# Kernel tuning notes

Measured on AMD Instinct MI355X. Metric: run time of the kernel, lower is better.

## Reference

```python
import jax, jax.numpy as jnp
import numpy as np


def conv3x3(x, w, b):
    # NCHW conv, 3x3, stride 1, pad 1
    y = jax.lax.conv_general_dilated(
        x, w, window_strides=(1, 1), padding=[(1, 1), (1, 1)],
        dimension_numbers=('NCHW', 'OIHW', 'NCHW'))
    return y + b[None, :, None, None]


def setup_inputs() -> dict:
    key = jax.random.key(0)
    ks = jax.random.split(key, 6)
    B, C, O, H, W = 4, 128, 128, 160, 160
    x = jax.random.normal(ks[0], (B, C, H, W), dtype=jnp.float32)
    # offset conv: small weights so sampling stays near the regular grid
    w_off = jax.random.normal(ks[1], (18, C, 3, 3), dtype=jnp.float32) * 0.1
    b_off = jnp.zeros((18,), dtype=jnp.float32)
    w_mask = jax.random.normal(ks[2], (9, C, 3, 3), dtype=jnp.float32) * 0.1
    b_mask = jnp.zeros((9,), dtype=jnp.float32)
    w = jax.random.normal(ks[3], (O, C, 3, 3), dtype=jnp.float32) * (1.0 / np.sqrt(C * 9))
    b = jax.random.normal(ks[4], (O,), dtype=jnp.float32) * 0.01
    return {'x': x, 'w_off': w_off, 'b_off': b_off,
            'w_mask': w_mask, 'b_mask': b_mask, 'w': w, 'b': b}


def reference(x, w_off, b_off, w_mask, b_mask, w, b):
    B, C, H, W = x.shape
    K = 9  # 3x3 kernel taps
    # offset: [B, 18, H, W] -> [B, K, 2, H, W]; channel layout is (dy, dx) per tap
    off = conv3x3(x, w_off, b_off).reshape(B, K, 2, H, W)
    dy, dx = off[:, :, 0], off[:, :, 1]                 # [B, K, H, W]
    mask = jax.nn.sigmoid(conv3x3(x, w_mask, b_mask))   # [B, K, H, W]

    # sampling positions: p = p_out - pad + k + offset  (stride 1, pad 1, dil 1)
    ky = (jnp.repeat(jnp.arange(3), 3) - 1).astype(x.dtype).reshape(1, K, 1, 1)
    kx = (jnp.tile(jnp.arange(3), 3) - 1).astype(x.dtype).reshape(1, K, 1, 1)
    hy = jnp.arange(H, dtype=x.dtype).reshape(1, 1, H, 1)
    wx = jnp.arange(W, dtype=x.dtype).reshape(1, 1, 1, W)
    py = hy + ky + dy   # [B, K, H, W]
    px = wx + kx + dx

    y0f = jnp.floor(py)
    x0f = jnp.floor(px)
    ly = py - y0f       # bilinear weights
    lx = px - x0f
    y0 = y0f.astype(jnp.int32)
    x0 = x0f.astype(jnp.int32)

    xf = x.reshape(B, C, H * W)

    def gather(iy, ix):
        # zero-padded gather at integer coords [B, K, H, W] -> [B, C, K, H, W]
        valid = ((iy >= 0) & (iy < H) & (ix >= 0) & (ix < W)).astype(x.dtype)
        idx = (jnp.clip(iy, 0, H - 1) * W + jnp.clip(ix, 0, W - 1)).reshape(B, 1, K * H * W)
        g = jnp.take_along_axis(xf, idx, axis=2).reshape(B, C, K, H, W)
        return g * valid[:, None]

    val = (gather(y0, x0) * ((1 - ly) * (1 - lx))[:, None]
           + gather(y0, x0 + 1) * ((1 - ly) * lx)[:, None]
           + gather(y0 + 1, x0) * (ly * (1 - lx))[:, None]
           + gather(y0 + 1, x0 + 1) * (ly * lx)[:, None])   # [B, C, K, H, W]

    val = val * mask[:, None]                                # modulated (DCNv2)
    out = jnp.einsum('bckhw,ock->bohw', val, w.reshape(w.shape[0], C, K))
    return out + b[None, :, None, None]
```

## Files before the change

kernel.cpp:

```cpp
#include <hip/hip_runtime.h>
#include <math.h>

constexpr int Bn = 4, Cc = 128, On = 128, Hh = 160, Ww = 160, Kk = 9;
constexpr int HW = Hh * Ww;

typedef __attribute__((ext_vector_type(8))) short s16x8;
typedef __attribute__((ext_vector_type(4))) float f32x4;

__device__ inline float bf2f(short s) {
    union { float f; unsigned u; } v;
    v.u = ((unsigned)(unsigned short)s) << 16;
    return v.f;
}
__device__ inline short f2bf(float f) {
    union { float f; unsigned u; } v;
    v.f = f;
    unsigned r = v.u + 0x7fffu + ((v.u >> 16) & 1u);
    return (short)(r >> 16);
}

__global__ __launch_bounds__(256) void to_nhwc(const float* __restrict__ x,
                                               short* __restrict__ xT,
                                               short* __restrict__ xLo) {
    __shared__ float tile[128][65];
    const int t = threadIdx.x;
    const int p0 = blockIdx.x * 64;
    const int b = blockIdx.y;
#pragma unroll
    for (int i = 0; i < 32; ++i) {
        int c = i * 4 + (t >> 6);
        tile[c][t & 63] = x[((size_t)b * Cc + c) * HW + p0 + (t & 63)];
    }
    __syncthreads();
    const int px = t >> 2, cq = t & 3;
    short* dsth = xT  + ((size_t)(b * HW) + p0 + px) * Cc;
    short* dstl = xLo + ((size_t)(b * HW) + p0 + px) * Cc;
#pragma unroll
    for (int j = 0; j < 8; ++j) {
        int c0 = cq * 4 + j * 16;
        short4 vh, vl;
        float f0 = tile[c0 + 0][px], f1 = tile[c0 + 1][px];
        float f2 = tile[c0 + 2][px], f3 = tile[c0 + 3][px];
        vh.x = f2bf(f0); vh.y = f2bf(f1); vh.z = f2bf(f2); vh.w = f2bf(f3);
        vl.x = f2bf(f0 - bf2f(vh.x));
        vl.y = f2bf(f1 - bf2f(vh.y));
        vl.z = f2bf(f2 - bf2f(vh.z));
        vl.w = f2bf(f3 - bf2f(vh.w));
        *(short4*)(dsth + c0) = vh;
        *(short4*)(dstl + c0) = vl;
    }
}

__global__ void prep_w(const float* __restrict__ wt, short* __restrict__ wb) {
    int idx = blockIdx.x * 256 + threadIdx.x;
    if (idx >= Kk * On * Cc) return;
    int c = idx & 127;
    int o = (idx >> 7) & 127;
    int k = idx >> 14;
    wb[idx] = f2bf(wt[(o * Cc + c) * 9 + k]);
}

__global__ void prep_wofm(const float* __restrict__ w_off,
                          const float* __restrict__ w_mask,
                          short* __restrict__ wh, short* __restrict__ wl) {
    int idx = blockIdx.x * 256 + threadIdx.x;
    if (idx >= Kk * 32 * Cc) return;
    int c = idx & 127;
    int ch = (idx >> 7) & 31;
    int k = idx >> 12;
    float v = 0.f;
    if (ch < 18)      v = w_off[(ch * Cc + c) * 9 + k];
    else if (ch < 27) v = w_mask[((ch - 18) * Cc + c) * 9 + k];
    short hi = f2bf(v);
    wh[idx] = hi;
    wl[idx] = f2bf(v - bf2f(hi));
}

__global__ __launch_bounds__(256) void offmask_mfma(
    const short* __restrict__ xT, const short* __restrict__ xLo,
    const short* __restrict__ wh, const short* __restrict__ wl,
    const float* __restrict__ b_off, const float* __restrict__ b_mask,
    float* __restrict__ dy_o, float* __restrict__ dx_o, float* __restrict__ mk_o)
{
    __shared__ short a_hi[6][2304];
    __shared__ short a_lo[6][2304];

    const int g = blockIdx.x;
    const int orig = (g & 7) * 200 + (g >> 3);
    const int b  = orig / 400;
    const int rem = orig % 400;
    const int h0 = (rem / 10) * 4;
    const int w0 = (rem % 10) * 16;

    const int t = threadIdx.x;

    const short* xh_b = xT  + (size_t)b * HW * Cc;
    const short* xl_b = xLo + (size_t)b * HW * Cc;
#pragma unroll
    for (int j = 0; j < 14; ++j) {
        int ci = j * 256 + t;
        if (ci < 3456) {
            int slot = ci / 576;
            int rem2 = ci % 576;
            int isLo = rem2 >= 288;
            int cj   = isLo ? rem2 - 288 : rem2;
            int pxl  = cj >> 4;
            int ck   = cj & 15;
            int r   = h0 - 1 + slot;
            int col = w0 - 1 + pxl;
            int4 v = make_int4(0, 0, 0, 0);
            if ((unsigned)r < (unsigned)Hh && (unsigned)col < (unsigned)Ww) {
                const short* src = (isLo ? xl_b : xh_b) +
                                   ((size_t)(r * Ww + col)) * Cc + ck * 8;
                v = *(const int4*)src;
            }
            int byte = (pxl * 256 + ck * 16) ^ ((pxl & 7) << 4);
            *(int4*)((char*)(isLo ? a_lo[slot] : a_hi[slot]) + byte) = v;
        }
    }
    __syncthreads();

    const int lane = t & 63, wid = t >> 6;
    const int i  = lane & 15;
    const int kb = (lane >> 4) * 8;

    f32x4 acc[2];
    acc[0] = (f32x4){0.f, 0.f, 0.f, 0.f};
    acc[1] = (f32x4){0.f, 0.f, 0.f, 0.f};

    s16x8 bh[2][2][4], bl[2][2][4];

#pragma unroll
    for (int tile = 0; tile < 2; ++tile) {
        const short* bp = wh + ((size_t)(tile * 16 + i)) * Cc + kb;
        const short* lp = wl + ((size_t)(tile * 16 + i)) * Cc + kb;
#pragma unroll
        for (int kk = 0; kk < 4; ++kk) {
            bh[0][tile][kk] = *(const s16x8*)(bp + kk * 32);
            bl[0][tile][kk] = *(const s16x8*)(lp + kk * 32);
        }
    }

#pragma unroll
    for (int k = 0; k < Kk; ++k) {
        const int cur = k & 1, nxt = cur ^ 1;
        if (k < Kk - 1) {
            const int kn = k + 1;
#pragma unroll
            for (int tile = 0; tile < 2; ++tile) {
                const short* bp = wh + ((size_t)(kn * 32 + tile * 16 + i)) * Cc + kb;
                const short* lp = wl + ((size_t)(kn * 32 + tile * 16 + i)) * Cc + kb;
#pragma unroll
                for (int kk = 0; kk < 4; ++kk) {
                    bh[nxt][tile][kk] = *(const s16x8*)(bp + kk * 32);
                    bl[nxt][tile][kk] = *(const s16x8*)(lp + kk * 32);
                }
            }
        }
        const int ky = k / 3, kxi = k % 3;
        const int slot = wid + ky;
        const int pxl = i + kxi;
        s16x8 ah[4], al[4];
#pragma unroll
        for (int kk = 0; kk < 4; ++kk) {
            int byte = (pxl * 256 + (kk * 32 + kb) * 2) ^ ((pxl & 7) << 4);
            ah[kk] = *(const s16x8*)((char*)a_hi[slot] + byte);
            al[kk] = *(const s16x8*)((char*)a_lo[slot] + byte);
        }
#pragma unroll
        for (int tile = 0; tile < 2; ++tile) {
#pragma unroll
            for (int kk = 0; kk < 4; ++kk) {
                acc[tile] = __builtin_amdgcn_mfma_f32_16x16x32_bf16(ah[kk], bh[cur][tile][kk], acc[tile], 0, 0, 0);
                acc[tile] = __builtin_amdgcn_mfma_f32_16x16x32_bf16(al[kk], bh[cur][tile][kk], acc[tile], 0, 0, 0);
                acc[tile] = __builtin_amdgcn_mfma_f32_16x16x32_bf16(ah[kk], bl[cur][tile][kk], acc[tile], 0, 0, 0);
            }
        }
    }

    const int hr = h0 + wid;
#pragma unroll
    for (int tile = 0; tile < 2; ++tile) {
        int ch = tile * 16 + i;
#pragma unroll
        for (int reg = 0; reg < 4; ++reg) {
            int pxo = (lane >> 4) * 4 + reg;
            int p = hr * Ww + w0 + pxo;
            float v = acc[tile][reg];
            if (ch < 18) {
                int k = ch >> 1;
                v += b_off[ch];
                if (ch & 1) dx_o[(size_t)(b * 9 + k) * HW + p] = v;
                else        dy_o[(size_t)(b * 9 + k) * HW + p] = v;
            } else if (ch < 27) {
                int k = ch - 18;
                v += b_mask[k];
                mk_o[(size_t)(b * 9 + k) * HW + p] = 1.f / (1.f + expf(-v));
            }
        }
    }
}

__global__ __launch_bounds__(256) void dconv_main(
    const short* __restrict__ xT,
    const short* __restrict__ wb,
    const float* __restrict__ bias,
    const float* __restrict__ dy_i, const float* __restrict__ dx_i,
    const float* __restrict__ mk_i,
    float* __restrict__ out)
{
    __shared__ short w_lds[2][128 * 128];

    const int g = blockIdx.x;
    const int orig = (g & 7) * 200 + (g >> 3);
    const int b = orig / 400;
    const int p0 = (orig % 400) * 64;

    const int t = threadIdx.x;
    const int lane = t & 63;
    const int wid = t >> 6;
    const int pm = wid * 16;

    const int myPx = pm + (lane & 15);
    const int p = p0 + myPx;
    const int h = p / Ww, w = p % Ww;
    const int kb8 = (lane >> 4) * 8;

    const short* xbase = xT + (size_t)b * HW * Cc + kb8;

    f32x4 acc[8];
#pragma unroll
    for (int i = 0; i < 8; ++i) acc[i] = (f32x4){0.f, 0.f, 0.f, 0.f};

    float wgbuf[2][4];
    int   idxc[4];
    s16x8 G[2][16];
    float omv[2][3];
    int4  Wr[8];

#define SETUP(kq, wbuf, dyv, dxv, mv)                                          \
    {                                                                          \
        float py  = (float)(h + ((kq) / 3) - 1) + (dyv);                       \
        float pxf = (float)(w + ((kq) % 3) - 1) + (dxv);                       \
        float y0f = floorf(py), x0f = floorf(pxf);                             \
        float ly = py - y0f, lx = pxf - x0f;                                   \
        int y0 = (int)y0f, x0 = (int)x0f;                                      \
        _Pragma("unroll")                                                      \
        for (int cr = 0; cr < 4; ++cr) {                                       \
            int iy = y0 + (cr >> 1), ix = x0 + (cr & 1);                       \
            bool ok = ((unsigned)iy < (unsigned)Hh) && ((unsigned)ix < (unsigned)Ww); \
            float wy = (cr >> 1) ? ly : (1.f - ly);                            \
            float wx = (cr & 1) ? lx : (1.f - lx);                             \
            int cy = min(max(iy, 0), Hh - 1);                                  \
            int cx = min(max(ix, 0), Ww - 1);                                  \
            idxc[cr] = cy * Ww + cx;                                           \
            wgbuf[wbuf][cr] = ok ? (wy * wx * (mv)) : 0.f;                     \
        }                                                                      \
    }

#define ISSUEG(gbuf)                                                           \
    {                                                                          \
        _Pragma("unroll")                                                      \
        for (int cr = 0; cr < 4; ++cr) {                                       \
            const short* src = xbase + (size_t)idxc[cr] * Cc;                  \
            _Pragma("unroll")                                                  \
            for (int kk = 0; kk < 4; ++kk)                                     \
                G[gbuf][cr * 4 + kk] = *(const s16x8*)(src + kk * 32);         \
        }                                                                      \
    }

#define LOADOM(kq, obuf)                                                       \
    {                                                                          \
        size_t ob = (size_t)(b * 9 + (kq)) * HW + p;                           \
        omv[obuf][0] = dy_i[ob]; omv[obuf][1] = dx_i[ob]; omv[obuf][2] = mk_i[ob]; \
    }

#define LOADW(kq)                                                              \
    {                                                                          \
        const int4* src = (const int4*)(wb + (size_t)(kq) * 128 * 128);        \
        _Pragma("unroll")                                                      \
        for (int i2 = 0; i2 < 8; ++i2) Wr[i2] = src[i2 * 256 + t];             \
    }

#define WRITEW(bufIdx)                                                         \
    {                                                                          \
        _Pragma("unroll")                                                      \
        for (int i2 = 0; i2 < 8; ++i2) {                                       \
            int ci = i2 * 256 + t;                                             \
            int o = ci >> 4;                                                   \
            int byte = (ci << 4) ^ ((o & 15) << 4);                            \
            *(int4*)((char*)w_lds[bufIdx] + byte) = Wr[i2];                    \
        }                                                                      \
    }

    LOADW(0);
    LOADOM(0, 0);
    LOADOM(1, 1);
    SETUP(0, 0, omv[0][0], omv[0][1], omv[0][2]);
    ISSUEG(0);
    WRITEW(0);
    __syncthreads();

#pragma unroll
    for (int k = 0; k < Kk; ++k) {
        if (k < Kk - 1) LOADW(k + 1);
        if (k < Kk - 2) LOADOM(k + 2, k & 1);
        if (k < Kk - 1) {
            SETUP(k + 1, (k + 1) & 1,
                  omv[(k + 1) & 1][0], omv[(k + 1) & 1][1], omv[(k + 1) & 1][2]);
            ISSUEG((k + 1) & 1);
        }

        s16x8 afr[4];
#pragma unroll
        for (int kk = 0; kk < 4; ++kk) {
#pragma unroll
            for (int j = 0; j < 8; ++j) {
                float sv = wgbuf[k & 1][0] * bf2f(G[k & 1][0 * 4 + kk][j])
                         + wgbuf[k & 1][1] * bf2f(G[k & 1][1 * 4 + kk][j])
                         + wgbuf[k & 1][2] * bf2f(G[k & 1][2 * 4 + kk][j])
                         + wgbuf[k & 1][3] * bf2f(G[k & 1][3 * 4 + kk][j]);
                afr[kk][j] = f2bf(sv);
            }
        }

        {
            const int orow = lane & 15;
#pragma unroll
            for (int ot = 0; ot < 8; ++ot) {
                int o = ot * 16 + orow;
#pragma unroll
                for (int kk = 0; kk < 4; ++kk) {
                    int byte = (o * 256 + (kk * 32 + kb8) * 2) ^ ((o & 15) << 4);
                    s16x8 bfr = *(const s16x8*)((char*)w_lds[k & 1] + byte);
                    acc[ot] = __builtin_amdgcn_mfma_f32_16x16x32_bf16(afr[kk], bfr, acc[ot], 0, 0, 0);
                }
            }
        }

        if (k < Kk - 1) WRITEW((k + 1) & 1);
        __syncthreads();
    }

#undef SETUP
#undef ISSUEG
#undef LOADOM
#undef LOADW
#undef WRITEW

#pragma unroll
    for (int ot = 0; ot < 8; ++ot) {
        int o = ot * 16 + (lane & 15);
        float bo = bias[o];
        float4 r;
        r.x = acc[ot][0] + bo;
        r.y = acc[ot][1] + bo;
        r.z = acc[ot][2] + bo;
        r.w = acc[ot][3] + bo;
        *(float4*)(out + ((size_t)(b * On + o)) * HW + p0 + pm + (lane >> 4) * 4) = r;
    }
}

extern "C" void kernel_launch(void* const* d_in, const int* in_sizes, int n_in,
                              void* d_out, int out_size, void* d_ws, size_t ws_size,
                              hipStream_t stream) {
    const float* x      = (const float*)d_in[0];
    const float* w_off  = (const float*)d_in[1];
    const float* b_off  = (const float*)d_in[2];
    const float* w_mask = (const float*)d_in[3];
    const float* b_mask = (const float*)d_in[4];
    const float* wt     = (const float*)d_in[5];
    const float* bias   = (const float*)d_in[6];
    float* out = (float*)d_out;

    short* xT  = (short*)d_ws;
    short* xLo = xT + (size_t)Bn * HW * Cc;
    short* wb  = xLo + (size_t)Bn * HW * Cc;
    short* wofm_h = wb + Kk * On * Cc;
    short* wofm_l = wofm_h + Kk * 32 * Cc;
    float* dy = (float*)(wofm_l + Kk * 32 * Cc);
    float* dx = dy + (size_t)Bn * 9 * HW;
    float* mk = dx + (size_t)Bn * 9 * HW;

    to_nhwc<<<dim3(HW / 64, Bn), 256, 0, stream>>>(x, xT, xLo);
    prep_w<<<(Kk * On * Cc + 255) / 256, 256, 0, stream>>>(wt, wb);
    prep_wofm<<<(Kk * 32 * Cc + 255) / 256, 256, 0, stream>>>(w_off, w_mask, wofm_h, wofm_l);
    offmask_mfma<<<1600, 256, 0, stream>>>(
        xT, xLo, wofm_h, wofm_l, b_off, b_mask, dy, dx, mk);
    dconv_main<<<1600, 256, 0, stream>>>(
        xT, wb, bias, dy, dx, mk, out);
}
```

Baseline: 303.5 us.

## Fuse offset/mask conv into deformable conv kernel via LDS staging

Merges the offset/mask convolution kernel into the main deformable conv kernel. Each block computes the 27 offset/mask channels for its 64 pixels with MFMA, reading x directly from global memory, and stores them in shared memory for the sampling setup. This drops one launch and the global write and read of the dy/dx/mask tensors. In exchange, the offset conv no longer stages a halo tile in LDS, so it uses uncached-pattern global loads per tap, and register and LDS pressure rise, which may lower occupancy.

```diff
diff --git a/kernel.cpp b/kernel.cpp
--- a/kernel.cpp
+++ b/kernel.cpp
@@ -3,6 +3,7 @@
 
 constexpr int Bn = 4, Cc = 128, On = 128, Hh = 160, Ww = 160, Kk = 9;
 constexpr int HW = Hh * Ww;
+constexpr int OMP = 69;
 
 typedef __attribute__((ext_vector_type(8))) short s16x8;
 typedef __attribute__((ext_vector_type(4))) float f32x4;
@@ -76,140 +77,18 @@
     wl[idx] = f2bf(v - bf2f(hi));
 }
 
-__global__ __launch_bounds__(256) void offmask_mfma(
-    const short* __restrict__ xT, const short* __restrict__ xLo,
-    const short* __restrict__ wh, const short* __restrict__ wl,
+__global__ __launch_bounds__(256) void dconv_fused(
+    const short* __restrict__ xT,
+    const short* __restrict__ xLo,
+    const short* __restrict__ wb,
+    const short* __restrict__ wh,
+    const short* __restrict__ wl,
     const float* __restrict__ b_off, const float* __restrict__ b_mask,
-    float* __restrict__ dy_o, float* __restrict__ dx_o, float* __restrict__ mk_o)
-{
-    __shared__ short a_hi[6][2304];
-    __shared__ short a_lo[6][2304];
-
-    const int g = blockIdx.x;
-    const int orig = (g & 7) * 200 + (g >> 3);
-    const int b  = orig / 400;
-    const int rem = orig % 400;
-    const int h0 = (rem / 10) * 4;
-    const int w0 = (rem % 10) * 16;
-
-    const int t = threadIdx.x;
-
-    const short* xh_b = xT  + (size_t)b * HW * Cc;
-    const short* xl_b = xLo + (size_t)b * HW * Cc;
-#pragma unroll
-    for (int j = 0; j < 14; ++j) {
-        int ci = j * 256 + t;
-        if (ci < 3456) {
-            int slot = ci / 576;
-            int rem2 = ci % 576;
-            int isLo = rem2 >= 288;
-            int cj   = isLo ? rem2 - 288 : rem2;
-            int pxl  = cj >> 4;
-            int ck   = cj & 15;
-            int r   = h0 - 1 + slot;
-            int col = w0 - 1 + pxl;
-            int4 v = make_int4(0, 0, 0, 0);
-            if ((unsigned)r < (unsigned)Hh && (unsigned)col < (unsigned)Ww) {
-                const short* src = (isLo ? xl_b : xh_b) +
-                                   ((size_t)(r * Ww + col)) * Cc + ck * 8;
-                v = *(const int4*)src;
-            }
-            int byte = (pxl * 256 + ck * 16) ^ ((pxl & 7) << 4);
-            *(int4*)((char*)(isLo ? a_lo[slot] : a_hi[slot]) + byte) = v;
-        }
-    }
-    __syncthreads();
-
-    const int lane = t & 63, wid = t >> 6;
-    const int i  = lane & 15;
-    const int kb = (lane >> 4) * 8;
-
-    f32x4 acc[2];
-    acc[0] = (f32x4){0.f, 0.f, 0.f, 0.f};
-    acc[1] = (f32x4){0.f, 0.f, 0.f, 0.f};
-
-    s16x8 bh[2][2][4], bl[2][2][4];
-
-#pragma unroll
-    for (int tile = 0; tile < 2; ++tile) {
-        const short* bp = wh + ((size_t)(tile * 16 + i)) * Cc + kb;
-        const short* lp = wl + ((size_t)(tile * 16 + i)) * Cc + kb;
-#pragma unroll
-        for (int kk = 0; kk < 4; ++kk) {
-            bh[0][tile][kk] = *(const s16x8*)(bp + kk * 32);
-            bl[0][tile][kk] = *(const s16x8*)(lp + kk * 32);
-        }
-    }
-
-#pragma unroll
-    for (int k = 0; k < Kk; ++k) {
-        const int cur = k & 1, nxt = cur ^ 1;
-        if (k < Kk - 1) {
-            const int kn = k + 1;
-#pragma unroll
-            for (int tile = 0; tile < 2; ++tile) {
-                const short* bp = wh + ((size_t)(kn * 32 + tile * 16 + i)) * Cc + kb;
-                const short* lp = wl + ((size_t)(kn * 32 + tile * 16 + i)) * Cc + kb;
-#pragma unroll
-                for (int kk = 0; kk < 4; ++kk) {
-                    bh[nxt][tile][kk] = *(const s16x8*)(bp + kk * 32);
-                    bl[nxt][tile][kk] = *(const s16x8*)(lp + kk * 32);
-                }
-            }
-        }
-        const int ky = k / 3, kxi = k % 3;
-        const int slot = wid + ky;
-        const int pxl = i + kxi;
-        s16x8 ah[4], al[4];
-#pragma unroll
-        for (int kk = 0; kk < 4; ++kk) {
-            int byte = (pxl * 256 + (kk * 32 + kb) * 2) ^ ((pxl & 7) << 4);
-            ah[kk] = *(const s16x8*)((char*)a_hi[slot] + byte);
-            al[kk] = *(const s16x8*)((char*)a_lo[slot] + byte);
-        }
-#pragma unroll
-        for (int tile = 0; tile < 2; ++tile) {
-#pragma unroll
-            for (int kk = 0; kk < 4; ++kk) {
-                acc[tile] = __builtin_amdgcn_mfma_f32_16x16x32_bf16(ah[kk], bh[cur][tile][kk], acc[tile], 0, 0, 0);
-                acc[tile] = __builtin_amdgcn_mfma_f32_16x16x32_bf16(al[kk], bh[cur][tile][kk], acc[tile], 0, 0, 0);
-                acc[tile] = __builtin_amdgcn_mfma_f32_16x16x32_bf16(ah[kk], bl[cur][tile][kk], acc[tile], 0, 0, 0);
-            }
-        }
-    }
-
-    const int hr = h0 + wid;
-#pragma unroll
-    for (int tile = 0; tile < 2; ++tile) {
-        int ch = tile * 16 + i;
-#pragma unroll
-        for (int reg = 0; reg < 4; ++reg) {
-            int pxo = (lane >> 4) * 4 + reg;
-            int p = hr * Ww + w0 + pxo;
-            float v = acc[tile][reg];
-            if (ch < 18) {
-                int k = ch >> 1;
-                v += b_off[ch];
-                if (ch & 1) dx_o[(size_t)(b * 9 + k) * HW + p] = v;
-                else        dy_o[(size_t)(b * 9 + k) * HW + p] = v;
-            } else if (ch < 27) {
-                int k = ch - 18;
-                v += b_mask[k];
-                mk_o[(size_t)(b * 9 + k) * HW + p] = 1.f / (1.f + expf(-v));
-            }
-        }
-    }
-}
-
-__global__ __launch_bounds__(256) void dconv_main(
-    const short* __restrict__ xT,
-    const short* __restrict__ wb,
     const float* __restrict__ bias,
-    const float* __restrict__ dy_i, const float* __restrict__ dx_i,
-    const float* __restrict__ mk_i,
     float* __restrict__ out)
 {
     __shared__ short w_lds[2][128 * 128];
+    __shared__ float om_lds[32 * OMP];
 
     const int g = blockIdx.x;
     const int orig = (g & 7) * 200 + (g >> 3);
@@ -221,12 +100,91 @@
     const int wid = t >> 6;
     const int pm = wid * 16;
 
-    const int myPx = pm + (lane & 15);
+    const int i16 = lane & 15;
+    const int myPx = pm + i16;
     const int p = p0 + myPx;
     const int h = p / Ww, w = p % Ww;
     const int kb8 = (lane >> 4) * 8;
 
-    const short* xbase = xT + (size_t)b * HW * Cc + kb8;
+    const short* xh_b = xT  + (size_t)b * HW * Cc;
+    const short* xl_b = xLo + (size_t)b * HW * Cc;
+    const short* xbase = xh_b + kb8;
+
+    const s16x8 vz = {0, 0, 0, 0, 0, 0, 0, 0};
+
+    {
+        f32x4 acc2[2];
+        acc2[0] = (f32x4){0.f, 0.f, 0.f, 0.f};
+        acc2[1] = (f32x4){0.f, 0.f, 0.f, 0.f};
+
+        s16x8 bhf[2][2][4], blf[2][2][4];
+#pragma unroll
+        for (int t2 = 0; t2 < 2; ++t2) {
+            const short* bp = wh + ((size_t)(t2 * 16 + i16)) * Cc + kb8;
+            const short* lp = wl + ((size_t)(t2 * 16 + i16)) * Cc + kb8;
+#pragma unroll
+            for (int kk = 0; kk < 4; ++kk) {
+                bhf[0][t2][kk] = *(const s16x8*)(bp + kk * 32);
+                blf[0][t2][kk] = *(const s16x8*)(lp + kk * 32);
+            }
+        }
+
+#pragma unroll
+        for (int k = 0; k < Kk; ++k) {
+            const int cur = k & 1, nxt = cur ^ 1;
+            if (k < Kk - 1) {
+                const int kn = k + 1;
+#pragma unroll
+                for (int t2 = 0; t2 < 2; ++t2) {
+                    const short* bp = wh + ((size_t)(kn * 32 + t2 * 16 + i16)) * Cc + kb8;
+                    const short* lp = wl + ((size_t)(kn * 32 + t2 * 16 + i16)) * Cc + kb8;
+#pragma unroll
+                    for (int kk = 0; kk < 4; ++kk) {
+                        bhf[nxt][t2][kk] = *(const s16x8*)(bp + kk * 32);
+                        blf[nxt][t2][kk] = *(const s16x8*)(lp + kk * 32);
+                    }
+                }
+            }
+            const int r  = h + (k / 3) - 1;
+            const int cl = w + (k % 3) - 1;
+            const bool ok = ((unsigned)r < (unsigned)Hh) && ((unsigned)cl < (unsigned)Ww);
+            const int rc = min(max(r, 0), Hh - 1) * Ww + min(max(cl, 0), Ww - 1);
+            const short* pa  = xh_b + (size_t)rc * Cc + kb8;
+            const short* pl2 = xl_b + (size_t)rc * Cc + kb8;
+            s16x8 ah[4], al[4];
+#pragma unroll
+            for (int kk = 0; kk < 4; ++kk) {
+                ah[kk] = *(const s16x8*)(pa + kk * 32);
+                al[kk] = *(const s16x8*)(pl2 + kk * 32);
+            }
+            if (!ok) {
+#pragma unroll
+                for (int kk = 0; kk < 4; ++kk) { ah[kk] = vz; al[kk] = vz; }
+            }
+#pragma unroll
+            for (int t2 = 0; t2 < 2; ++t2) {
+#pragma unroll
+                for (int kk = 0; kk < 4; ++kk) {
+                    acc2[t2] = __builtin_amdgcn_mfma_f32_16x16x32_bf16(ah[kk], bhf[cur][t2][kk], acc2[t2], 0, 0, 0);
+                    acc2[t2] = __builtin_amdgcn_mfma_f32_16x16x32_bf16(al[kk], bhf[cur][t2][kk], acc2[t2], 0, 0, 0);
+                    acc2[t2] = __builtin_amdgcn_mfma_f32_16x16x32_bf16(ah[kk], blf[cur][t2][kk], acc2[t2], 0, 0, 0);
+                }
+            }
+        }
+
+#pragma unroll
+        for (int t2 = 0; t2 < 2; ++t2) {
+            int ch = t2 * 16 + i16;
+#pragma unroll
+            for (int reg = 0; reg < 4; ++reg) {
+                int pxl = pm + (lane >> 4) * 4 + reg;
+                float v = acc2[t2][reg];
+                if (ch < 18)       v += b_off[ch];
+                else if (ch < 27)  v = 1.f / (1.f + expf(-(v + b_mask[ch - 18])));
+                om_lds[ch * OMP + pxl] = v;
+            }
+        }
+    }
 
     f32x4 acc[8];
 #pragma unroll
@@ -235,13 +193,15 @@
     float wgbuf[2][4];
     int   idxc[4];
     s16x8 G[2][16];
-    float omv[2][3];
     int4  Wr[8];
 
-#define SETUP(kq, wbuf, dyv, dxv, mv)                                          \
+#define SETUP(kq, wbuf)                                                        \
     {                                                                          \
-        float py  = (float)(h + ((kq) / 3) - 1) + (dyv);                       \
-        float pxf = (float)(w + ((kq) % 3) - 1) + (dxv);                       \
+        float dyv = om_lds[(2 * (kq)) * OMP + myPx];                           \
+        float dxv = om_lds[(2 * (kq) + 1) * OMP + myPx];                       \
+        float mv  = om_lds[(18 + (kq)) * OMP + myPx];                          \
+        float py  = (float)(h + ((kq) / 3) - 1) + dyv;                         \
+        float pxf = (float)(w + ((kq) % 3) - 1) + dxv;                         \
         float y0f = floorf(py), x0f = floorf(pxf);                             \
         float ly = py - y0f, lx = pxf - x0f;                                   \
         int y0 = (int)y0f, x0 = (int)x0f;                                      \
@@ -254,7 +214,7 @@
             int cy = min(max(iy, 0), Hh - 1);                                  \
             int cx = min(max(ix, 0), Ww - 1);                                  \
             idxc[cr] = cy * Ww + cx;                                           \
-            wgbuf[wbuf][cr] = ok ? (wy * wx * (mv)) : 0.f;                     \
+            wgbuf[wbuf][cr] = ok ? (wy * wx * mv) : 0.f;                       \
         }                                                                      \
     }
 
@@ -269,12 +229,6 @@
         }                                                                      \
     }
 
-#define LOADOM(kq, obuf)                                                       \
-    {                                                                          \
-        size_t ob = (size_t)(b * 9 + (kq)) * HW + p;                           \
-        omv[obuf][0] = dy_i[ob]; omv[obuf][1] = dx_i[ob]; omv[obuf][2] = mk_i[ob]; \
-    }
-
 #define LOADW(kq)                                                              \
     {                                                                          \
         const int4* src = (const int4*)(wb + (size_t)(kq) * 128 * 128);        \
@@ -294,9 +248,7 @@
     }
 
     LOADW(0);
-    LOADOM(0, 0);
-    LOADOM(1, 1);
-    SETUP(0, 0, omv[0][0], omv[0][1], omv[0][2]);
+    SETUP(0, 0);
     ISSUEG(0);
     WRITEW(0);
     __syncthreads();
@@ -304,10 +256,8 @@
 #pragma unroll
     for (int k = 0; k < Kk; ++k) {
         if (k < Kk - 1) LOADW(k + 1);
-        if (k < Kk - 2) LOADOM(k + 2, k & 1);
         if (k < Kk - 1) {
-            SETUP(k + 1, (k + 1) & 1,
-                  omv[(k + 1) & 1][0], omv[(k + 1) & 1][1], omv[(k + 1) & 1][2]);
+            SETUP(k + 1, (k + 1) & 1);
             ISSUEG((k + 1) & 1);
         }
 
@@ -344,7 +294,6 @@
 
 #undef SETUP
 #undef ISSUEG
-#undef LOADOM
 #undef LOADW
 #undef WRITEW
 
@@ -378,15 +327,10 @@
     short* wb  = xLo + (size_t)Bn * HW * Cc;
     short* wofm_h = wb + Kk * On * Cc;
     short* wofm_l = wofm_h + Kk * 32 * Cc;
-    float* dy = (float*)(wofm_l + Kk * 32 * Cc);
-    float* dx = dy + (size_t)Bn * 9 * HW;
-    float* mk = dx + (size_t)Bn * 9 * HW;
 
     to_nhwc<<<dim3(HW / 64, Bn), 256, 0, stream>>>(x, xT, xLo);
     prep_w<<<(Kk * On * Cc + 255) / 256, 256, 0, stream>>>(wt, wb);
     prep_wofm<<<(Kk * 32 * Cc + 255) / 256, 256, 0, stream>>>(w_off, w_mask, wofm_h, wofm_l);
-    offmask_mfma<<<1600, 256, 0, stream>>>(
-        xT, xLo, wofm_h, wofm_l, b_off, b_mask, dy, dx, mk);
-    dconv_main<<<1600, 256, 0, stream>>>(
-        xT, wb, bias, dy, dx, mk, out);
-}
+    dconv_fused<<<1600, 256, 0, stream>>>(
+        xT, xLo, wb, wofm_h, wofm_l, b_off, b_mask, bias, out);
+}
```

After: 327.2 us. +7.8%, slower.
